# Optimization experiments

Measured on AMD Instinct MI355X. Metric: run time of the kernel, lower is better.

The kernel has to match this reference:

```python
import jax, jax.numpy as jnp
import numpy as np

B, PQ, C, NH, L, P, FF = 8, 900, 256, 8, 4, 4, 2048
SHAPES = [(100, 152), (50, 76), (25, 38), (13, 19)]
PK = sum(h * w for h, w in SHAPES)
DH = C // NH


def setup_inputs() -> dict:
    key = jax.random.key(0)
    ks = jax.random.split(key, 20)
    s = 0.02
    w = lambda i, shp: jax.random.normal(ks[i], shp, jnp.float32) * s
    starts = np.cumsum([0] + [h * wd for h, wd in SHAPES[:-1]]).astype(np.int64)
    return dict(
        query=w(0, (B, C, PQ)),
        key=w(1, (B, C, PK)),
        query_pos=jax.random.uniform(ks[2], (B, PQ, 3)),
        key_pos=jax.random.uniform(ks[3], (B, PK, 3)),
        reference_points=jax.random.uniform(ks[4], (B, PQ, L, 2)),
        W_in=w(5, (3 * C, C)), b_in=jnp.zeros(3 * C),
        W_out=w(6, (C, C)), b_out=jnp.zeros(C),
        W_off=w(7, (NH * L * P * 2, C)),
        b_off=jax.random.uniform(ks[8], (NH * L * P * 2,), minval=-1.0, maxval=1.0),
        W_aw=w(9, (NH * L * P, C)), b_aw=jnp.zeros(NH * L * P),
        W_v=w(10, (C, C)), b_v=jnp.zeros(C),
        W_o=w(11, (C, C)), b_o=jnp.zeros(C),
        W1=w(12, (FF, C)), b1=jnp.zeros(FF),
        W2=w(13, (C, FF)), b2=jnp.zeros(C),
        g1=jnp.ones(C), be1=jnp.zeros(C),
        g2=jnp.ones(C), be2=jnp.zeros(C),
        g3=jnp.ones(C), be3=jnp.zeros(C),
        spatial_shapes=np.array(SHAPES, np.int64),
        level_start_index=starts,
    )


def layer_norm(x, g, b):
    m = x.mean(-1, keepdims=True)
    v = x.var(-1, keepdims=True)
    return (x - m) * jax.lax.rsqrt(v + 1e-5) * g + b


def mha(x, W_in, b_in, W_out, b_out):
    # x: [S, B, C]; torch nn.MultiheadAttention with q=k=v=x
    S, Bn, _ = x.shape
    qkv = x @ W_in.T + b_in
    q, k, v = jnp.split(qkv, 3, axis=-1)
    to_h = lambda t: t.reshape(S, Bn, NH, DH).transpose(1, 2, 0, 3)  # [B,H,S,Dh]
    q, k, v = to_h(q), to_h(k), to_h(v)
    attn = jax.nn.softmax(jnp.einsum('bhqd,bhkd->bhqk', q, k) / np.sqrt(DH), axis=-1)
    o = jnp.einsum('bhqk,bhkd->bhqd', attn, v).transpose(2, 0, 1, 3).reshape(S, Bn, C)
    return o @ W_out.T + b_out


def ms_deform(value, loc, aw, shapes, starts):
    # value [B,PK,NH,DH], loc [B,PQ,NH,L,P,2] in [0,1], aw [B,PQ,NH,L,P]
    v = value.transpose(0, 2, 1, 3)          # [B,NH,PK,DH]
    locT = loc.transpose(0, 2, 1, 3, 4, 5)   # [B,NH,PQ,L,P,2]
    awT = aw.transpose(0, 2, 1, 3, 4)        # [B,NH,PQ,L,P]
    out = jnp.zeros((B, NH, PQ, DH), value.dtype)
    for l, (Hl, Wl) in enumerate(shapes):
        st = starts[l]
        vl = v[:, :, st:st + Hl * Wl]        # [B,NH,Hl*Wl,DH]
        x = locT[..., l, :, 0] * Wl - 0.5    # [B,NH,PQ,P]  (align_corners=False)
        y = locT[..., l, :, 1] * Hl - 0.5
        x0 = jnp.floor(x); y0 = jnp.floor(y)
        lw, lh = x - x0, y - y0
        x0i = x0.astype(jnp.int32); y0i = y0.astype(jnp.int32)

        def gather(ix, iy):
            valid = ((ix >= 0) & (ix < Wl) & (iy >= 0) & (iy < Hl)).astype(vl.dtype)
            idx = jnp.clip(iy, 0, Hl - 1) * Wl + jnp.clip(ix, 0, Wl - 1)
            g = jnp.take_along_axis(vl, idx.reshape(B, NH, -1, 1), axis=2)
            return g.reshape(B, NH, PQ, P, DH) * valid[..., None]

        samp = (gather(x0i, y0i) * ((1 - lw) * (1 - lh))[..., None]
                + gather(x0i + 1, y0i) * (lw * (1 - lh))[..., None]
                + gather(x0i, y0i + 1) * ((1 - lw) * lh)[..., None]
                + gather(x0i + 1, y0i + 1) * (lw * lh)[..., None])  # [B,NH,PQ,P,DH]
        out = out + (samp * awT[..., l, :, None]).sum(3)
    return out.transpose(0, 2, 1, 3).reshape(B, PQ, C)


def reference(query, key, query_pos, key_pos, reference_points,
              W_in, b_in, W_out, b_out, W_off, b_off, W_aw, b_aw,
              W_v, b_v, W_o, b_o, W1, b1, W2, b2,
              g1, be1, g2, be2, g3, be3,
              spatial_shapes, level_start_index):
    shapes = [tuple(int(t) for t in r) for r in np.asarray(spatial_shapes)]
    starts = [int(t) for t in np.asarray(level_start_index)]
    q = query.transpose(2, 0, 1)   # [PQ,B,C]
    k = key.transpose(2, 0, 1)     # [PK,B,C]
    # self-attention (posembeds are None in this config)
    q = layer_norm(q + mha(q, W_in, b_in, W_out, b_out), g1, be1)
    # multi-scale deformable cross-attention
    qd = q.transpose(1, 0, 2)      # [B,PQ,C]
    kf = k.transpose(1, 0, 2)      # [B,PK,C]
    value = (kf @ W_v.T + b_v).reshape(B, PK, NH, DH)
    off = (qd @ W_off.T + b_off).reshape(B, PQ, NH, L, P, 2)
    aw = jax.nn.softmax((qd @ W_aw.T + b_aw).reshape(B, PQ, NH, L * P), -1)
    aw = aw.reshape(B, PQ, NH, L, P)
    norm = jnp.asarray([[w_, h_] for (h_, w_) in shapes], jnp.float32)  # [L,2] as (W,H)
    loc = reference_points[:, :, None, :, None, :] + off / norm[None, None, None, :, None, :]
    q2 = ms_deform(value, loc, aw, shapes, starts) @ W_o.T + b_o
    q = layer_norm(q + q2.transpose(1, 0, 2), g2, be2)
    # FFN
    ff = jax.nn.relu(q @ W1.T + b1) @ W2.T + b2
    q = layer_norm(q + ff, g3, be3)
    return q.transpose(1, 2, 0)    # [B,C,PQ]
```

## Files before the change

### kernel.cpp

```cpp
#include <hip/hip_runtime.h>
#include <hip/hip_bf16.h>
#include <stdint.h>

typedef __hip_bfloat16 bf16;
typedef short bf16x8 __attribute__((ext_vector_type(8)));
typedef short s4v    __attribute__((ext_vector_type(4)));
typedef float f32x4  __attribute__((ext_vector_type(4)));

constexpr int B_  = 8;
constexpr int PQ_ = 900;
constexpr int C_  = 256;
constexpr int NH_ = 8;
constexpr int L_  = 4;
constexpr int P_  = 4;
constexpr int FF_ = 2048;
constexpr int DH_ = 32;
constexpr int PK_ = 20197;
constexpr int VLD = 960;

__device__ __forceinline__ short f2b(float f) {
    __hip_bfloat16 h = __float2bfloat16(f);
    union { __hip_bfloat16 h; short s; } u; u.h = h; return u.s;
}
__device__ __forceinline__ float b2f(short s) {
    union { short s; __hip_bfloat16 h; } u; u.s = s; return __bfloat162float(u.h);
}

__launch_bounds__(256)
__global__ void wcvt_kernel(const float* __restrict__ p0, const float* __restrict__ p1,
                            const float* __restrict__ p2, const float* __restrict__ p3,
                            const float* __restrict__ p4, const float* __restrict__ p5,
                            const float* __restrict__ p6, const float* __restrict__ p7,
                            short* __restrict__ dst)
{
    const int g = (blockIdx.x * 256 + threadIdx.x) * 4;
    const float* src; int off;
    if      (g < 196608)  { src = p0; off = 0; }
    else if (g < 262144)  { src = p1; off = 196608; }
    else if (g < 327680)  { src = p2; off = 262144; }
    else if (g < 360448)  { src = p3; off = 327680; }
    else if (g < 425984)  { src = p4; off = 360448; }
    else if (g < 491520)  { src = p5; off = 425984; }
    else if (g < 1015808) { src = p6; off = 491520; }
    else                  { src = p7; off = 1015808; }
    float4 v = *(const float4*)(src + (g - off));
    s4v pk = {f2b(v.x), f2b(v.y), f2b(v.z), f2b(v.w)};
    *(s4v*)&dst[g] = pk;
}

__launch_bounds__(512)
__global__ void vgemm3_kernel(const float* __restrict__ key, const short* __restrict__ Wv,
                              const float* __restrict__ bias, short* __restrict__ value,
                              int Mb)
{
    constexpr int CST = 40;
    __shared__ short Sh[8 * 64 * CST];
    short* As = Sh;

    const int tid = threadIdx.x;
    const int wv = tid >> 6, lane = tid & 63;
    const int quad = lane >> 4, lrow = lane & 15;

    const int m0 = blockIdx.x * 64;
    const int gm = m0 + lane;
    const bool va = gm < Mb;
    int b = 0, s = 0;
    if (va) { b = gm / PK_; s = gm - b * PK_; }
    const int64_t rbase = (int64_t)(b * 256) * PK_ + s;

#pragma unroll
    for (int jj = 0; jj < 4; ++jj) {
        short pk[8];
#pragma unroll
        for (int j = 0; j < 8; ++j) {
            const int c = wv * 32 + jj * 8 + j;
            pk[j] = f2b(va ? key[rbase + (int64_t)c * PK_] : 0.f);
        }
        const int slot = wv * 4 + jj;
        const int phys = (slot + lane) & 31;
        *(bf16x8*)&As[lane * 256 + phys * 8] = *(const bf16x8*)pk;
    }
    __syncthreads();

    float bia[2];
#pragma unroll
    for (int nf = 0; nf < 2; ++nf) bia[nf] = bias[wv * 32 + nf * 16 + lrow];

    f32x4 acc[4][2];
#pragma unroll
    for (int mf = 0; mf < 4; ++mf)
#pragma unroll
        for (int nf = 0; nf < 2; ++nf) acc[mf][nf] = (f32x4){0.f, 0.f, 0.f, 0.f};

#pragma unroll
    for (int kh = 0; kh < 8; ++kh) {
        bf16x8 a[4];
#pragma unroll
        for (int mf = 0; mf < 4; ++mf) {
            const int r = mf * 16 + lrow;
            const int phys = ((kh * 4 + quad) + r) & 31;
            a[mf] = *(const bf16x8*)&As[r * 256 + phys * 8];
        }
        bf16x8 wf[2];
#pragma unroll
        for (int nf = 0; nf < 2; ++nf)
            wf[nf] = *(const bf16x8*)&Wv[(int64_t)(wv * 32 + nf * 16 + lrow) * 256 + kh * 32 + quad * 8];
#pragma unroll
        for (int mf = 0; mf < 4; ++mf)
#pragma unroll
            for (int nf = 0; nf < 2; ++nf)
                acc[mf][nf] = __builtin_amdgcn_mfma_f32_16x16x32_bf16(a[mf], wf[nf], acc[mf][nf], 0, 0, 0);
    }
    __syncthreads();

    short* Cs = &Sh[wv * 64 * CST];
#pragma unroll
    for (int nf = 0; nf < 2; ++nf)
#pragma unroll
        for (int mf = 0; mf < 4; ++mf)
#pragma unroll
            for (int r = 0; r < 4; ++r)
                Cs[(mf * 16 + quad * 4 + r) * CST + nf * 16 + lrow] = f2b(acc[mf][nf][r] + bia[nf]);
#pragma unroll
    for (int jj = 0; jj < 4; ++jj) {
        const int row = (lane >> 2) + jj * 16;
        const int rr = m0 + row;
        bf16x8 pk = *(const bf16x8*)&Cs[row * CST + (lane & 3) * 8];
        if (rr < Mb)
            *(bf16x8*)&value[(int64_t)rr * 256 + wv * 32 + (lane & 3) * 8] = pk;
    }
}

template <int NF, bool DBUF, bool AF32, bool WF32, bool CF32, bool RELU>
__launch_bounds__(256)
__global__ void mfma_gemm(const void* __restrict__ Ap, const void* __restrict__ Wp,
                          const float* __restrict__ bias, void* __restrict__ Cp,
                          int Mb, int N, int K, int tilesM,
                          int ldA, int ldW, int ldC, int nbI,
                          int64_t sAo, int64_t sAi, int64_t sWo, int64_t sWi,
                          int64_t sCo, int64_t sCi, float scale)
{
    constexpr int BN  = 64 * NF;
    constexpr int LDR = 72;
    constexpr int NB  = DBUF ? 2 : 1;
    __shared__ short As[NB * 64 * LDR];
    __shared__ short Ws[NB * BN * LDR];

    const int tid   = threadIdx.x;
    const int batch = blockIdx.y / tilesM;
    const int m0    = (blockIdx.y % tilesM) * 64;
    const int n0    = blockIdx.x * BN;
    const int outer = batch / nbI, inner = batch % nbI;
    const int64_t offA = (int64_t)outer * sAo + (int64_t)inner * sAi;
    const int64_t offW = (int64_t)outer * sWo + (int64_t)inner * sWi;
    const int64_t offC = (int64_t)outer * sCo + (int64_t)inner * sCi;

    const int w = tid >> 6, lane = tid & 63;
    const int quad = lane >> 4, lrow = lane & 15;
    const int colbase = n0 + w * 16 * NF;

    const int sm  = tid >> 2;
    const int skb = (tid & 3) * 16;

    const int T = (K + 63) / 64;

    bf16x8 areg[2];
    bf16x8 wreg[2 * NF];

    auto stageA = [&](int t) {
        const int k0 = t * 64;
        const int gm = m0 + sm;
#pragma unroll
        for (int c = 0; c < 2; ++c) {
            const int k = k0 + skb + c * 8;
            bf16x8 pk = {0, 0, 0, 0, 0, 0, 0, 0};
            if (gm < Mb && k + 8 <= K) {
                if (AF32) {
                    const float* s = (const float*)Ap + offA + (int64_t)gm * ldA + k;
                    float4 u0 = *(const float4*)s;
                    float4 u1 = *(const float4*)(s + 4);
                    pk = (bf16x8){f2b(u0.x), f2b(u0.y), f2b(u0.z), f2b(u0.w),
                                  f2b(u1.x), f2b(u1.y), f2b(u1.z), f2b(u1.w)};
                } else {
                    pk = *(const bf16x8*)((const short*)Ap + offA + (int64_t)gm * ldA + k);
                }
            }
            areg[c] = pk;
        }
    };
    auto stageW = [&](int t) {
        const int k0 = t * 64;
#pragma unroll
        for (int j = 0; j < NF; ++j) {
            const int gn = n0 + j * 64 + sm;
#pragma unroll
            for (int c = 0; c < 2; ++c) {
                const int k = k0 + skb + c * 8;
                bf16x8 pk = {0, 0, 0, 0, 0, 0, 0, 0};
                if (gn < N && k + 8 <= K) {
                    if (WF32) {
                        const float* s = (const float*)Wp + offW + (int64_t)gn * ldW + k;
                        float4 u0 = *(const float4*)s;
                        float4 u1 = *(const float4*)(s + 4);
                        pk = (bf16x8){f2b(u0.x), f2b(u0.y), f2b(u0.z), f2b(u0.w),
                                      f2b(u1.x), f2b(u1.y), f2b(u1.z), f2b(u1.w)};
                    } else {
                        pk = *(const bf16x8*)((const short*)Wp + offW + (int64_t)gn * ldW + k);
                    }
                }
                wreg[j * 2 + c] = pk;
            }
        }
    };
    auto writeLDS = [&](int buf) {
#pragma unroll
        for (int c = 0; c < 2; ++c)
            *(bf16x8*)&As[(buf * 64 + sm) * LDR + skb + c * 8] = areg[c];
#pragma unroll
        for (int j = 0; j < NF; ++j)
#pragma unroll
            for (int c = 0; c < 2; ++c)
                *(bf16x8*)&Ws[(buf * BN + j * 64 + sm) * LDR + skb + c * 8] = wreg[j * 2 + c];
    };

    f32x4 acc[4][NF];
#pragma unroll
    for (int i = 0; i < 4; ++i)
#pragma unroll
        for (int j = 0; j < NF; ++j) acc[i][j] = (f32x4){0.f, 0.f, 0.f, 0.f};

    auto compute = [&](int buf) {
        bf16x8 a[4][2], bb[NF][2];
#pragma unroll
        for (int kh = 0; kh < 2; ++kh) {
#pragma unroll
            for (int mf = 0; mf < 4; ++mf)
                a[mf][kh] = *(const bf16x8*)&As[(buf * 64 + mf * 16 + lrow) * LDR + kh * 32 + quad * 8];
#pragma unroll
            for (int nf = 0; nf < NF; ++nf)
                bb[nf][kh] = *(const bf16x8*)&Ws[(buf * BN + w * 16 * NF + nf * 16 + lrow) * LDR + kh * 32 + quad * 8];
        }
#pragma unroll
        for (int kh = 0; kh < 2; ++kh)
#pragma unroll
            for (int mf = 0; mf < 4; ++mf)
#pragma unroll
                for (int nf = 0; nf < NF; ++nf)
                    acc[mf][nf] = __builtin_amdgcn_mfma_f32_16x16x32_bf16(a[mf][kh], bb[nf][kh], acc[mf][nf], 0, 0, 0);
    };

    if (DBUF) {
        stageA(0); stageW(0); writeLDS(0);
        __syncthreads();
        for (int t = 0; t < T; ++t) {
            const int cur = t & 1;
            if (t + 1 < T) { stageA(t + 1); stageW(t + 1); }
            compute(cur);
            if (t + 1 < T) {
                writeLDS(cur ^ 1);
                __syncthreads();
            }
        }
    } else {
        for (int t = 0; t < T; ++t) {
            stageA(t); stageW(t);
            if (t > 0) __syncthreads();
            writeLDS(0);
            __syncthreads();
            compute(0);
        }
    }

#pragma unroll
    for (int nf = 0; nf < NF; ++nf) {
        const int col = colbase + nf * 16 + lrow;
        if (col >= N) continue;
        const float bia = bias ? bias[col] : 0.f;
#pragma unroll
        for (int mf = 0; mf < 4; ++mf) {
            const int row0 = m0 + mf * 16 + quad * 4;
#pragma unroll
            for (int r = 0; r < 4; ++r) {
                const int rr = row0 + r;
                if (rr < Mb) {
                    float v = acc[mf][nf][r] * scale + bia;
                    if (RELU) v = fmaxf(v, 0.f);
                    const int64_t idx = offC + (int64_t)rr * ldC + col;
                    if (CF32) ((float*)Cp)[idx] = v;
                    else      ((short*)Cp)[idx] = f2b(v);
                }
            }
        }
    }
}

template <int NF, bool DBUF, bool AF32, bool WF32, bool CF32, bool RELU>
static void mfma_launch(const void* A, const void* W, const float* bias, void* Cp,
                        int nb, int nbI, int Mb, int N, int K,
                        int ldA, int ldW, int ldC,
                        int64_t sAo, int64_t sAi, int64_t sWo, int64_t sWi,
                        int64_t sCo, int64_t sCi, float scale, hipStream_t stream)
{
    int tilesM = (Mb + 63) / 64;
    dim3 grid((N + 64 * NF - 1) / (64 * NF), nb * tilesM);
    mfma_gemm<NF, DBUF, AF32, WF32, CF32, RELU><<<grid, 256, 0, stream>>>(
        A, W, bias, Cp, Mb, N, K, tilesM, ldA, ldW, ldC, nbI,
        sAo, sAi, sWo, sWi, sCo, sCi, scale);
}

__launch_bounds__(256)
__global__ void transpose_kernel(const float* __restrict__ src, short* __restrict__ dst,
                                 int Scount, int ldS, int64_t sbs, int64_t dbs)
{
    const int tid = threadIdx.x;
    const int b = blockIdx.z;
    const int s0 = blockIdx.x * 32, c0 = blockIdx.y * 32;
    __shared__ float t[32][33];
    {
        const int c_l = tid >> 3, sq = (tid & 7) * 4;
        const int64_t base = (int64_t)b * sbs + (int64_t)(c0 + c_l) * ldS;
#pragma unroll
        for (int i = 0; i < 4; ++i) {
            const int s = s0 + sq + i;
            t[c_l][sq + i] = (s < Scount) ? src[base + s] : 0.f;
        }
    }
    __syncthreads();
    {
        const int s_l = tid >> 3, cq = (tid & 7) * 4;
        const int s = s0 + s_l;
        if (s < Scount) {
            s4v pk = {f2b(t[cq + 0][s_l]), f2b(t[cq + 1][s_l]),
                      f2b(t[cq + 2][s_l]), f2b(t[cq + 3][s_l])};
            *(s4v*)&dst[(int64_t)b * dbs + (int64_t)s * 256 + c0 + cq] = pk;
        }
    }
}

__launch_bounds__(256)
__global__ void vt_kernel(const short* __restrict__ qkv, short* __restrict__ VT)
{
    const int tid = threadIdx.x;
    const int bh = blockIdx.y, b = bh >> 3, h = bh & 7;
    const int s0 = blockIdx.x * 32;
    __shared__ short t[32][36];
    {
        const int s_l = tid >> 3, dq = (tid & 7) * 4;
        const int s = s0 + s_l;
        s4v pk = {0, 0, 0, 0};
        if (s < 900)
            pk = *(const s4v*)&qkv[((int64_t)(b * 900 + s)) * 768 + 512 + h * 32 + dq];
        *(s4v*)&t[s_l][dq] = pk;
    }
    __syncthreads();
    {
        const int d = tid >> 3, sq = (tid & 7) * 4;
        s4v pk = {t[sq + 0][d], t[sq + 1][d], t[sq + 2][d], t[sq + 3][d]};
        *(s4v*)&VT[((int64_t)bh * 32 + d) * VLD + s0 + sq] = pk;
    }
}

__launch_bounds__(256)
__global__ void attn_fused(const short* __restrict__ qkv, const short* __restrict__ VT,
                           short* __restrict__ attno)
{
    __shared__ short Pl[4 * 16 * 72];
    const int tid = threadIdx.x;
    const int wv = tid >> 6, lane = tid & 63;
    const int quad = lane >> 4, lrow = lane & 15;
    const int bh = blockIdx.y, b = bh >> 3, h = bh & 7;
    const int q0 = blockIdx.x * 64 + wv * 16;
    const float iscale = 0.17677669529663687f;

    bf16x8 aq = {0, 0, 0, 0, 0, 0, 0, 0};
    {
        const int q = q0 + lrow;
        if (q < 900)
            aq = *(const bf16x8*)&qkv[((int64_t)(b * 900 + q)) * 768 + h * 32 + quad * 8];
    }

    float mrow[4], lsum[4];
    f32x4 o[2] = {{0.f, 0.f, 0.f, 0.f}, {0.f, 0.f, 0.f, 0.f}};
#pragma unroll
    for (int r = 0; r < 4; ++r) { mrow[r] = -1e30f; lsum[r] = 0.f; }

    short* Pw = &Pl[wv * 16 * 72];

    for (int st = 0; st < 15; ++st) {
        const int s0 = st * 64;
        f32x4 sc[4];
#pragma unroll
        for (int nf = 0; nf < 4; ++nf) {
            const int s = s0 + nf * 16 + lrow;
            bf16x8 kb = {0, 0, 0, 0, 0, 0, 0, 0};
            if (s < 900)
                kb = *(const bf16x8*)&qkv[((int64_t)(b * 900 + s)) * 768 + 256 + h * 32 + quad * 8];
            sc[nf] = __builtin_amdgcn_mfma_f32_16x16x32_bf16(aq, kb, (f32x4){0.f, 0.f, 0.f, 0.f}, 0, 0, 0);
        }
#pragma unroll
        for (int nf = 0; nf < 4; ++nf) {
            const int s = s0 + nf * 16 + lrow;
            if (s >= 900) sc[nf] = (f32x4){-1e30f, -1e30f, -1e30f, -1e30f};
            else {
#pragma unroll
                for (int r = 0; r < 4; ++r) sc[nf][r] *= iscale;
            }
        }
        float alpha[4], ps[4][4], rsum[4];
#pragma unroll
        for (int r = 0; r < 4; ++r) {
            float tm = fmaxf(fmaxf(sc[0][r], sc[1][r]), fmaxf(sc[2][r], sc[3][r]));
#pragma unroll
            for (int off = 1; off < 16; off <<= 1)
                tm = fmaxf(tm, __shfl_xor(tm, off, 64));
            const float nm = fmaxf(mrow[r], tm);
            alpha[r] = __expf(mrow[r] - nm);
            mrow[r] = nm;
            float s4 = 0.f;
#pragma unroll
            for (int nf = 0; nf < 4; ++nf) {
                const float p = __expf(sc[nf][r] - nm);
                ps[nf][r] = p;
                s4 += p;
            }
#pragma unroll
            for (int off = 1; off < 16; off <<= 1)
                s4 += __shfl_xor(s4, off, 64);
            rsum[r] = s4;
        }
#pragma unroll
        for (int nf2 = 0; nf2 < 2; ++nf2)
#pragma unroll
            for (int r = 0; r < 4; ++r) o[nf2][r] *= alpha[r];
#pragma unroll
        for (int r = 0; r < 4; ++r) lsum[r] = lsum[r] * alpha[r] + rsum[r];
#pragma unroll
        for (int nf = 0; nf < 4; ++nf)
#pragma unroll
            for (int r = 0; r < 4; ++r)
                Pw[(quad * 4 + r) * 72 + nf * 16 + lrow] = f2b(ps[nf][r]);
#pragma unroll
        for (int kh = 0; kh < 2; ++kh) {
            bf16x8 pa = *(const bf16x8*)&Pw[lrow * 72 + kh * 32 + quad * 8];
#pragma unroll
            for (int nf2 = 0; nf2 < 2; ++nf2) {
                const int d = nf2 * 16 + lrow;
                bf16x8 vb = *(const bf16x8*)&VT[((int64_t)bh * 32 + d) * VLD + s0 + kh * 32 + quad * 8];
                o[nf2] = __builtin_amdgcn_mfma_f32_16x16x32_bf16(pa, vb, o[nf2], 0, 0, 0);
            }
        }
    }
#pragma unroll
    for (int r = 0; r < 4; ++r) {
        const int q = q0 + quad * 4 + r;
        if (q < 900) {
            const float inv = 1.f / lsum[r];
#pragma unroll
            for (int nf2 = 0; nf2 < 2; ++nf2)
                attno[((int64_t)(b * 900 + q)) * 256 + h * 32 + nf2 * 16 + lrow] = f2b(o[nf2][r] * inv);
        }
    }
}

template <int MODE>
__launch_bounds__(256)
__global__ void ln_kernel(const float* __restrict__ y, const void* __restrict__ res,
                          const float* __restrict__ g, const float* __restrict__ be,
                          float* __restrict__ out_f, short* __restrict__ out_b)
{
    const int bt = blockIdx.x;
    const int b = bt / PQ_, t = bt % PQ_;
    const int c = threadIdx.x;
    const int wv = c >> 6, lane = c & 63;

    float r;
    if (MODE == 0)      r = ((const float*)res)[((int64_t)b * C_ + c) * PQ_ + t];
    else if (MODE == 1) r = ((const float*)res)[(int64_t)bt * C_ + c];
    else                r = b2f(((const short*)res)[(int64_t)bt * C_ + c]);
    const float v = r + y[(int64_t)bt * C_ + c];

    __shared__ float p1[4], p2[4];
    float a = v, sq = v * v;
#pragma unroll
    for (int off = 32; off > 0; off >>= 1) {
        a  += __shfl_xor(a, off, 64);
        sq += __shfl_xor(sq, off, 64);
    }
    if (lane == 0) { p1[wv] = a; p2[wv] = sq; }
    __syncthreads();
    const float s1 = p1[0] + p1[1] + p1[2] + p1[3];
    const float s2 = p2[0] + p2[1] + p2[2] + p2[3];
    const float mean = s1 * (1.f / C_);
    const float var  = s2 * (1.f / C_) - mean * mean;
    const float o = (v - mean) * rsqrtf(var + 1e-5f) * g[c] + be[c];

    if (MODE == 0) { out_f[(int64_t)bt * C_ + c] = o; out_b[(int64_t)bt * C_ + c] = f2b(o); }
    else if (MODE == 1) out_b[(int64_t)bt * C_ + c] = f2b(o);
    else out_f[((int64_t)b * C_ + c) * PQ_ + t] = o;
}

__launch_bounds__(256)
__global__ void deform_kernel(const float* __restrict__ offb, const float* __restrict__ awl,
                              const float* __restrict__ refp, const short* __restrict__ value,
                              short* __restrict__ samp)
{
    const int half = threadIdx.x >> 7;
    const int t = threadIdx.x & 127;
    const int bt = blockIdx.x * 2 + half;
    const int b = bt / PQ_;
    const int h = t >> 4, dp = t & 15;

    __shared__ float Loff[2][256];
    __shared__ float Law[2][128];
    __shared__ float Lref[2][8];

    Loff[half][t]       = offb[(int64_t)bt * 256 + t];
    Loff[half][t + 128] = offb[(int64_t)bt * 256 + t + 128];
    Law[half][t]        = awl[(int64_t)bt * 128 + t];
    if (t < 8) Lref[half][t] = refp[(int64_t)bt * 8 + t];
    __syncthreads();

    float m = -1e30f;
#pragma unroll
    for (int i = 0; i < 16; ++i) m = fmaxf(m, Law[half][h * 16 + i]);
    float s = 0.f;
#pragma unroll
    for (int i = 0; i < 16; ++i) s += __expf(Law[half][h * 16 + i] - m);
    const float invs = 1.f / s;

    const int HLc[4] = {100, 50, 25, 13};
    const int WLc[4] = {152, 76, 38, 19};
    const int STc[4] = {0, 15200, 19000, 19950};

    float acc0 = 0.f, acc1 = 0.f;
#pragma unroll
    for (int l = 0; l < L_; ++l) {
        const int Hl = HLc[l], Wl = WLc[l], st0 = STc[l];
        const float fx = Lref[half][l * 2 + 0], fy = Lref[half][l * 2 + 1];
#pragma unroll
        for (int p = 0; p < P_; ++p) {
            const float ox = Loff[half][h * 32 + l * 8 + p * 2 + 0];
            const float oy = Loff[half][h * 32 + l * 8 + p * 2 + 1];
            const float x = (fx + ox / (float)Wl) * (float)Wl - 0.5f;
            const float y = (fy + oy / (float)Hl) * (float)Hl - 0.5f;
            const float x0f = floorf(x), y0f = floorf(y);
            const int x0 = (int)x0f, y0 = (int)y0f;
            const float lw = x - x0f, lh = y - y0f;
            const float w00 = (1.f - lw) * (1.f - lh), w10 = lw * (1.f - lh);
            const float w01 = (1.f - lw) * lh,         w11 = lw * lh;
            const float aww = __expf(Law[half][h * 16 + l * 4 + p] - m) * invs;

            float sv0 = 0.f, sv1 = 0.f;
            int ix, iy; float w;
#pragma unroll
            for (int cidx = 0; cidx < 4; ++cidx) {
                if (cidx == 0) { ix = x0;     iy = y0;     w = w00; }
                if (cidx == 1) { ix = x0 + 1; iy = y0;     w = w10; }
                if (cidx == 2) { ix = x0;     iy = y0 + 1; w = w01; }
                if (cidx == 3) { ix = x0 + 1; iy = y0 + 1; w = w11; }
                if (ix >= 0 && ix < Wl && iy >= 0 && iy < Hl) {
                    const int64_t vi = ((int64_t)(b * PK_ + st0 + iy * Wl + ix)) * 256 + h * 32 + dp * 2;
                    const uint32_t pr = *(const uint32_t*)&value[vi];
                    sv0 += w * b2f((short)(pr & 0xffff));
                    sv1 += w * b2f((short)(pr >> 16));
                }
            }
            acc0 += sv0 * aww;
            acc1 += sv1 * aww;
        }
    }
    union { uint32_t u; short s2[2]; } o;
    o.s2[0] = f2b(acc0);
    o.s2[1] = f2b(acc1);
    *(uint32_t*)&samp[(int64_t)bt * 256 + h * 32 + dp * 2] = o.u;
}

extern "C" void kernel_launch(void* const* d_in, const int* in_sizes, int n_in,
                              void* d_out, int out_size, void* d_ws, size_t ws_size,
                              hipStream_t stream)
{
    const float* query = (const float*)d_in[0];
    const float* key   = (const float*)d_in[1];
    const float* refp  = (const float*)d_in[4];
    const float* W_in  = (const float*)d_in[5];
    const float* b_in  = (const float*)d_in[6];
    const float* W_out = (const float*)d_in[7];
    const float* b_out = (const float*)d_in[8];
    const float* W_off = (const float*)d_in[9];
    const float* b_off = (const float*)d_in[10];
    const float* W_aw  = (const float*)d_in[11];
    const float* b_aw  = (const float*)d_in[12];
    const float* W_v   = (const float*)d_in[13];
    const float* b_v   = (const float*)d_in[14];
    const float* W_o   = (const float*)d_in[15];
    const float* b_o   = (const float*)d_in[16];
    const float* W1    = (const float*)d_in[17];
    const float* b1    = (const float*)d_in[18];
    const float* W2    = (const float*)d_in[19];
    const float* b2    = (const float*)d_in[20];
    const float* g1    = (const float*)d_in[21];
    const float* be1   = (const float*)d_in[22];
    const float* g2    = (const float*)d_in[23];
    const float* be2   = (const float*)d_in[24];
    const float* g3    = (const float*)d_in[25];
    const float* be3   = (const float*)d_in[26];

    char* X  = (char*)d_ws;
    char* Yb = X + 62259200;
    char* Z1 = Yb + 7372800;
    char* Wa = Z1 + 7372800;
    char* Wb_ = Wa + 3686400;
    char* VA = Wb_ + 3686400;
    char* WB = VA + 82726912;

    short* qkvb   = (short*)X;
    short* queryT = (short*)(X + 11059200);
    short* VT     = (short*)(X + 14745600);
    short* attno  = (short*)(X + 18677760);
    short* ffh    = (short*)X;
    float* proj   = (float*)Yb;
    float* offb   = (float*)Yb;
    float* proj2  = (float*)Yb;
    float* ffo    = (float*)Yb;
    float* q1     = (float*)Z1;
    short* q1b    = (short*)Wa;
    short* samp   = (short*)Wa;
    float* awl    = (float*)Wb_;
    short* q2nb   = (short*)Wb_;
    short* value  = (short*)VA;

    short* WBs    = (short*)WB;
    short* Wb_in  = WBs;
    short* Wb_out = WBs + 196608;
    short* Wb_off = WBs + 262144;
    short* Wb_aw  = WBs + 327680;
    short* Wb_v   = WBs + 360448;
    short* Wb_o   = WBs + 425984;
    short* Wb1    = WBs + 491520;
    short* Wb2    = WBs + 1015808;

    wcvt_kernel<<<1504, 256, 0, stream>>>(W_in, W_out, W_off, W_aw, W_v, W_o, W1, W2, WBs);
    transpose_kernel<<<dim3(29, 8, B_), 256, 0, stream>>>(query, queryT, PQ_, PQ_,
                                                          (int64_t)C_ * PQ_, (int64_t)PQ_ * C_);
    mfma_launch<1, true, false, false, false, false>(queryT, Wb_in, b_in, qkvb, 1, 1, B_ * PQ_, 768, 256,
                                                     256, 256, 768, 0, 0, 0, 0, 0, 0, 1.f, stream);
    vt_kernel<<<dim3(30, 64), 256, 0, stream>>>(qkvb, VT);
    attn_fused<<<dim3(15, 64), 256, 0, stream>>>(qkvb, VT, attno);
    mfma_launch<1, true, false, false, true, false>(attno, Wb_out, b_out, proj, 1, 1, B_ * PQ_, 256, 256,
                                                    256, 256, 256, 0, 0, 0, 0, 0, 0, 1.f, stream);
    ln_kernel<0><<<B_ * PQ_, 256, 0, stream>>>(proj, query, g1, be1, q1, q1b);
    mfma_launch<1, true, false, false, true, false>(q1b, Wb_off, b_off, offb, 1, 1, B_ * PQ_, 256, 256,
                                                    256, 256, 256, 0, 0, 0, 0, 0, 0, 1.f, stream);
    mfma_launch<1, true, false, false, true, false>(q1b, Wb_aw, b_aw, awl, 1, 1, B_ * PQ_, 128, 256,
                                                    256, 256, 128, 0, 0, 0, 0, 0, 0, 1.f, stream);
    vgemm3_kernel<<<(B_ * PK_ + 63) / 64, 512, 0, stream>>>(key, Wb_v, b_v, value, B_ * PK_);
    deform_kernel<<<B_ * PQ_ / 2, 256, 0, stream>>>(offb, awl, refp, value, samp);
    mfma_launch<1, true, false, false, true, false>(samp, Wb_o, b_o, proj2, 1, 1, B_ * PQ_, 256, 256,
                                                    256, 256, 256, 0, 0, 0, 0, 0, 0, 1.f, stream);
    ln_kernel<1><<<B_ * PQ_, 256, 0, stream>>>(proj2, q1, g2, be2, nullptr, q2nb);
    mfma_launch<1, true, false, false, false, true>(q2nb, Wb1, b1, ffh, 1, 1, B_ * PQ_, FF_, 256,
                                                    256, 256, FF_, 0, 0, 0, 0, 0, 0, 1.f, stream);
    mfma_launch<1, true, false, false, true, false>(ffh, Wb2, b2, ffo, 1, 1, B_ * PQ_, 256, FF_,
                                                    FF_, FF_, 256, 0, 0, 0, 0, 0, 0, 1.f, stream);
    ln_kernel<2><<<B_ * PQ_, 256, 0, stream>>>(ffo, q2nb, g3, be3, (float*)d_out, nullptr);

    (void)in_sizes; (void)n_in; (void)out_size; (void)ws_size;
}
```

Measured before the change: 641.1 us.

## Merge offset/attention-weight GEMMs and split-K the FFN down-projection into LayerNorm

The offset and attention-weight projections now run as one GEMM with N=384, relying on W_aw being stored right after W_off in the bf16 weight buffer and using a second bias for columns past 256. The deform kernel reads both from the single combined buffer. The FFN second GEMM (K=2048) is split into four K=512 partial GEMMs, which gives more blocks for parallelism. Their fp32 partials are summed together with b2 inside the final LayerNorm kernel. This adds extra fp32 partial-buffer traffic and workspace in exchange for fewer launches and better occupancy on the long-K GEMM.

After: 637.5 us. About the same (-0.6%).

```diff
diff --git a/kernel.cpp b/kernel.cpp
--- a/kernel.cpp
+++ b/kernel.cpp
@@ -17,6 +17,7 @@
 constexpr int DH_ = 32;
 constexpr int PK_ = 20197;
 constexpr int VLD = 960;
+constexpr int64_t FFS = (int64_t)B_ * PQ_ * C_;
 
 __device__ __forceinline__ short f2b(float f) {
     __hip_bfloat16 h = __float2bfloat16(f);
@@ -138,7 +139,8 @@
                           int Mb, int N, int K, int tilesM,
                           int ldA, int ldW, int ldC, int nbI,
                           int64_t sAo, int64_t sAi, int64_t sWo, int64_t sWi,
-                          int64_t sCo, int64_t sCi, float scale)
+                          int64_t sCo, int64_t sCi, float scale,
+                          const float* __restrict__ bias2, int nsplit)
 {
     constexpr int BN  = 64 * NF;
     constexpr int LDR = 72;
@@ -275,7 +277,9 @@
     for (int nf = 0; nf < NF; ++nf) {
         const int col = colbase + nf * 16 + lrow;
         if (col >= N) continue;
-        const float bia = bias ? bias[col] : 0.f;
+        float bia;
+        if (col < nsplit) bia = bias ? bias[col] : 0.f;
+        else              bia = bias2[col - nsplit];
 #pragma unroll
         for (int mf = 0; mf < 4; ++mf) {
             const int row0 = m0 + mf * 16 + quad * 4;
@@ -299,13 +303,14 @@
                         int nb, int nbI, int Mb, int N, int K,
                         int ldA, int ldW, int ldC,
                         int64_t sAo, int64_t sAi, int64_t sWo, int64_t sWi,
-                        int64_t sCo, int64_t sCi, float scale, hipStream_t stream)
+                        int64_t sCo, int64_t sCi, float scale, hipStream_t stream,
+                        const float* bias2 = nullptr, int nsplit = 1 << 30)
 {
     int tilesM = (Mb + 63) / 64;
     dim3 grid((N + 64 * NF - 1) / (64 * NF), nb * tilesM);
     mfma_gemm<NF, DBUF, AF32, WF32, CF32, RELU><<<grid, 256, 0, stream>>>(
         A, W, bias, Cp, Mb, N, K, tilesM, ldA, ldW, ldC, nbI,
-        sAo, sAi, sWo, sWi, sCo, sCi, scale);
+        sAo, sAi, sWo, sWi, sCo, sCi, scale, bias2, nsplit);
 }
 
 __launch_bounds__(256)
@@ -466,7 +471,8 @@
 __launch_bounds__(256)
 __global__ void ln_kernel(const float* __restrict__ y, const void* __restrict__ res,
                           const float* __restrict__ g, const float* __restrict__ be,
-                          float* __restrict__ out_f, short* __restrict__ out_b)
+                          float* __restrict__ out_f, short* __restrict__ out_b,
+                          const float* __restrict__ eb)
 {
     const int bt = blockIdx.x;
     const int b = bt / PQ_, t = bt % PQ_;
@@ -477,7 +483,17 @@
     if (MODE == 0)      r = ((const float*)res)[((int64_t)b * C_ + c) * PQ_ + t];
     else if (MODE == 1) r = ((const float*)res)[(int64_t)bt * C_ + c];
     else                r = b2f(((const short*)res)[(int64_t)bt * C_ + c]);
-    const float v = r + y[(int64_t)bt * C_ + c];
+
+    float yv;
+    if (MODE == 2) {
+        yv = eb[c];
+#pragma unroll
+        for (int i = 0; i < 4; ++i)
+            yv += y[(int64_t)i * FFS + (int64_t)bt * C_ + c];
+    } else {
+        yv = y[(int64_t)bt * C_ + c];
+    }
+    const float v = r + yv;
 
     __shared__ float p1[4], p2[4];
     float a = v, sq = v * v;
@@ -500,7 +516,7 @@
 }
 
 __launch_bounds__(256)
-__global__ void deform_kernel(const float* __restrict__ offb, const float* __restrict__ awl,
+__global__ void deform_kernel(const float* __restrict__ oa,
                               const float* __restrict__ refp, const short* __restrict__ value,
                               short* __restrict__ samp)
 {
@@ -514,9 +530,9 @@
     __shared__ float Law[2][128];
     __shared__ float Lref[2][8];
 
-    Loff[half][t]       = offb[(int64_t)bt * 256 + t];
-    Loff[half][t + 128] = offb[(int64_t)bt * 256 + t + 128];
-    Law[half][t]        = awl[(int64_t)bt * 128 + t];
+    Loff[half][t]       = oa[(int64_t)bt * 384 + t];
+    Loff[half][t + 128] = oa[(int64_t)bt * 384 + t + 128];
+    Law[half][t]        = oa[(int64_t)bt * 384 + 256 + t];
     if (t < 8) Lref[half][t] = refp[(int64_t)bt * 8 + t];
     __syncthreads();
 
@@ -612,6 +628,8 @@
     char* Wb_ = Wa + 3686400;
     char* VA = Wb_ + 3686400;
     char* WB = VA + 82726912;
+    char* OA = WB + 3080192;
+    char* FFP = OA + 11059200;
 
     short* qkvb   = (short*)X;
     short* queryT = (short*)(X + 11059200);
@@ -619,21 +637,18 @@
     short* attno  = (short*)(X + 18677760);
     short* ffh    = (short*)X;
     float* proj   = (float*)Yb;
-    float* offb   = (float*)Yb;
-    float* proj2  = (float*)Yb;
-    float* ffo    = (float*)Yb;
     float* q1     = (float*)Z1;
     short* q1b    = (short*)Wa;
     short* samp   = (short*)Wa;
-    float* awl    = (float*)Wb_;
     short* q2nb   = (short*)Wb_;
     short* value  = (short*)VA;
+    float* oa     = (float*)OA;
+    float* ffp    = (float*)FFP;
 
     short* WBs    = (short*)WB;
     short* Wb_in  = WBs;
     short* Wb_out = WBs + 196608;
     short* Wb_off = WBs + 262144;
-    short* Wb_aw  = WBs + 327680;
     short* Wb_v   = WBs + 360448;
     short* Wb_o   = WBs + 425984;
     short* Wb1    = WBs + 491520;
@@ -648,21 +663,21 @@
     attn_fused<<<dim3(15, 64), 256, 0, stream>>>(qkvb, VT, attno);
     mfma_launch<1, true, false, false, true, false>(attno, Wb_out, b_out, proj, 1, 1, B_ * PQ_, 256, 256,
                                                     256, 256, 256, 0, 0, 0, 0, 0, 0, 1.f, stream);
-    ln_kernel<0><<<B_ * PQ_, 256, 0, stream>>>(proj, query, g1, be1, q1, q1b);
-    mfma_launch<1, true, false, false, true, false>(q1b, Wb_off, b_off, offb, 1, 1, B_ * PQ_, 256, 256,
+    ln_kernel<0><<<B_ * PQ_, 256, 0, stream>>>(proj, query, g1, be1, q1, q1b, nullptr);
+    mfma_launch<1, true, false, false, true, false>(q1b, Wb_off, b_off, oa, 1, 1, B_ * PQ_, 384, 256,
+                                                    256, 256, 384, 0, 0, 0, 0, 0, 0, 1.f, stream,
+                                                    b_aw, 256);
+    vgemm3_kernel<<<(B_ * PK_ + 63) / 64, 512, 0, stream>>>(key, Wb_v, b_v, value, B_ * PK_);
+    deform_kernel<<<B_ * PQ_ / 2, 256, 0, stream>>>(oa, refp, value, samp);
+    mfma_launch<1, true, false, false, true, false>(samp, Wb_o, b_o, proj, 1, 1, B_ * PQ_, 256, 256,
                                                     256, 256, 256, 0, 0, 0, 0, 0, 0, 1.f, stream);
-    mfma_launch<1, true, false, false, true, false>(q1b, Wb_aw, b_aw, awl, 1, 1, B_ * PQ_, 128, 256,
-                                                    256, 256, 128, 0, 0, 0, 0, 0, 0, 1.f, stream);
-    vgemm3_kernel<<<(B_ * PK_ + 63) / 64, 512, 0, stream>>>(key, Wb_v, b_v, value, B_ * PK_);
-    deform_kernel<<<B_ * PQ_ / 2, 256, 0, stream>>>(offb, awl, refp, value, samp);
-    mfma_launch<1, true, false, false, true, false>(samp, Wb_o, b_o, proj2, 1, 1, B_ * PQ_, 256, 256,
-                                                    256, 256, 256, 0, 0, 0, 0, 0, 0, 1.f, stream);
-    ln_kernel<1><<<B_ * PQ_, 256, 0, stream>>>(proj2, q1, g2, be2, nullptr, q2nb);
+    ln_kernel<1><<<B_ * PQ_, 256, 0, stream>>>(proj, q1, g2, be2, nullptr, q2nb, nullptr);
     mfma_launch<1, true, false, false, false, true>(q2nb, Wb1, b1, ffh, 1, 1, B_ * PQ_, FF_, 256,
                                                     256, 256, FF_, 0, 0, 0, 0, 0, 0, 1.f, stream);
-    mfma_launch<1, true, false, false, true, false>(ffh, Wb2, b2, ffo, 1, 1, B_ * PQ_, 256, FF_,
-                                                    FF_, FF_, 256, 0, 0, 0, 0, 0, 0, 1.f, stream);
-    ln_kernel<2><<<B_ * PQ_, 256, 0, stream>>>(ffo, q2nb, g3, be3, (float*)d_out, nullptr);
+    mfma_launch<1, true, false, false, true, false>(ffh, Wb2, nullptr, ffp, 4, 1, B_ * PQ_, 256, 512,
+                                                    FF_, FF_, 256,
+                                                    512, 0, 512, 0, FFS, 0, 1.f, stream);
+    ln_kernel<2><<<B_ * PQ_, 256, 0, stream>>>(ffp, q2nb, g3, be3, (float*)d_out, nullptr, b2);
 
     (void)in_sizes; (void)n_in; (void)out_size; (void)ws_size;
 }
```
